# Kernel tuning notes

Hardware: AMD Instinct MI355X
Metric: run time of the kernel (lower is better)

The kernel has to match this reference:

```python
import jax, jax.numpy as jnp
import numpy as np

GAMMA = 1.0
INF_REPLACE = 1e10  # original code replaces inf with 1e10 before logsumexp


def _softmin3(r_diag, r_up, r_left, gamma):
    # softmin over the 3 DP neighbors (stack order matches original: diag, up, left)
    x = jnp.stack([r_diag, r_up, r_left], axis=0)  # (3, B)
    x = jnp.where(jnp.isinf(x), jnp.asarray(INF_REPLACE, x.dtype), x)
    return -gamma * jax.nn.logsumexp(-x / gamma, axis=0)  # (B,)


def _cdist(X, Y):
    # Euclidean pairwise distance, torch.cdist(p=2): (B,N,d),(B,M,d) -> (B,N,M)
    d2 = (jnp.sum(X * X, axis=-1)[:, :, None]
          + jnp.sum(Y * Y, axis=-1)[:, None, :]
          - 2.0 * jnp.einsum('bnd,bmd->bnm', X, Y))
    return jnp.sqrt(jnp.maximum(d2, 0.0))


def _soft_dtw(X, Y, gamma):
    B, N, _ = X.shape
    D = _cdist(X, Y)  # (B, N, N)
    inf = jnp.asarray(jnp.inf, D.dtype)

    # R row 0: [0, inf, inf, ...] per batch
    prev_row0 = jnp.full((B, N + 1), inf, dtype=D.dtype).at[:, 0].set(0.0)

    def row_step(prev_row, d_row):
        # prev_row: (B, N+1) = R[i-1, :]; d_row: (B, N) = D[:, i-1, :]
        xs = (d_row.T, prev_row[:, :-1].T, prev_row[:, 1:].T)  # each (N, B)

        def col_step(r_left, x):
            d, r_diag, r_up = x  # each (B,)
            r = d + _softmin3(r_diag, r_up, r_left, gamma)
            return r, r

        _, row = jax.lax.scan(col_step, jnp.full((B,), inf, dtype=D.dtype), xs)
        new_row = jnp.concatenate([jnp.full((B, 1), inf, dtype=D.dtype), row.T], axis=1)
        return new_row, None

    last_row, _ = jax.lax.scan(row_step, prev_row0, jnp.swapaxes(D, 0, 1))
    return last_row[:, -1]  # R[:, N, N], shape (B,)


def setup_inputs() -> dict:
    key = jax.random.key(0)
    kx, ky = jax.random.split(key)
    B, N, d = 64, 512, 64
    X = jax.random.normal(kx, (B, N, d), dtype=jnp.float32)
    Y = jax.random.normal(ky, (B, N, d), dtype=jnp.float32)
    return {"X": X, "Y": Y}


def reference(X, Y):
    return _soft_dtw(X, Y, GAMMA)
```

## Files before the change

### kernel.cpp

```cpp
#include <hip/hip_runtime.h>
#include <math.h>

#define NB 64
#define NN 512
#define ND 64

#define LOG2E 1.4426950408889634f
#define LN2   0.6931471805599453f
#define RING  16
#define NINF  __int_as_float(0xFF800000u)

typedef __attribute__((ext_vector_type(8))) short  bf16x8;
typedef __attribute__((ext_vector_type(4))) float  f32x4;

static __device__ __forceinline__ unsigned short f2bf(float f) {
    unsigned u = __float_as_uint(f);
    u += 0x7FFFu + ((u >> 16) & 1u);
    return (unsigned short)(u >> 16);
}

__global__ __launch_bounds__(256) void cdist_kernel(const float* __restrict__ X,
                                                    const float* __restrict__ Y,
                                                    unsigned short* __restrict__ Wt) {
    __shared__ unsigned short lX[8][2][512];
    __shared__ unsigned short lY[8][2][512];
    __shared__ float nrmX[128], nrmY[128];

    const int b  = blockIdx.z;
    const int ib = blockIdx.x * 128;
    const int jb = blockIdx.y * 128;
    const int t  = threadIdx.x;

    {
        const int r = t & 127;
        const float* src = (t < 128) ? X + ((size_t)b * NN + ib + r) * ND
                                     : Y + ((size_t)b * NN + jb + r) * ND;
        float v[ND];
        float s = 0.f;
        #pragma unroll
        for (int k = 0; k < ND; k += 4) {
            float4 f = *(const float4*)(src + k);
            v[k] = f.x; v[k + 1] = f.y; v[k + 2] = f.z; v[k + 3] = f.w;
            s += f.x * f.x + f.y * f.y + f.z * f.z + f.w * f.w;
        }
        const int it = r >> 4;
        const int lm = r & 15;
        unsigned short* dst = (t < 128) ? &lX[it][0][0] : &lY[it][0][0];
        #pragma unroll
        for (int h = 0; h < 2; ++h) {
            #pragma unroll
            for (int q = 0; q < 4; ++q) {
                unsigned w[4];
                #pragma unroll
                for (int m = 0; m < 4; ++m) {
                    const int c = h * 32 + q * 8 + 2 * m;
                    w[m] = (unsigned)f2bf(v[c]) | ((unsigned)f2bf(v[c + 1]) << 16);
                }
                uint4 pkt; pkt.x = w[0]; pkt.y = w[1]; pkt.z = w[2]; pkt.w = w[3];
                *(uint4*)(dst + h * 512 + (q * 16 + lm) * 8) = pkt;
            }
        }
        if (t < 128) nrmX[r] = s; else nrmY[r] = s;
    }
    __syncthreads();

    const int wave = t >> 6;
    const int wi   = (wave & 1) * 64;
    const int wj   = (wave >> 1) * 64;
    const int lane = t & 63;
    const int lm   = lane & 15;
    const int quad = lane >> 4;

    f32x4 acc[4][4];
    #pragma unroll
    for (int mt = 0; mt < 4; ++mt)
        #pragma unroll
        for (int nt = 0; nt < 4; ++nt)
            acc[mt][nt] = (f32x4){0.f, 0.f, 0.f, 0.f};

    const int jt0 = wj >> 4;
    const int it0 = wi >> 4;

    #pragma unroll
    for (int h = 0; h < 2; ++h) {
        bf16x8 Af[4], Bf[4];
        #pragma unroll
        for (int mt = 0; mt < 4; ++mt)
            Af[mt] = *(const bf16x8*)&lY[jt0 + mt][h][lane * 8];
        #pragma unroll
        for (int nt = 0; nt < 4; ++nt)
            Bf[nt] = *(const bf16x8*)&lX[it0 + nt][h][lane * 8];
        #pragma unroll
        for (int mt = 0; mt < 4; ++mt)
            #pragma unroll
            for (int nt = 0; nt < 4; ++nt)
                acc[mt][nt] = __builtin_amdgcn_mfma_f32_16x16x32_bf16(
                    Af[mt], Bf[nt], acc[mt][nt], 0, 0, 0);
    }

    float nxv[4];
    float4 nyv[4];
    #pragma unroll
    for (int nt = 0; nt < 4; ++nt)
        nxv[nt] = nrmX[wi + nt * 16 + lm];
    #pragma unroll
    for (int mt = 0; mt < 4; ++mt)
        nyv[mt] = *(const float4*)&nrmY[wj + mt * 16 + quad * 4];

    #pragma unroll
    for (int nt = 0; nt < 4; ++nt) {
        const int i = ib + wi + nt * 16 + lm;
        unsigned short* Drow = Wt + ((size_t)b * NN + i) * NN + jb + wj;
        #pragma unroll
        for (int mt = 0; mt < 4; ++mt) {
            const float* nyp = (const float*)&nyv[mt];
            unsigned a[4];
            #pragma unroll
            for (int r = 0; r < 4; ++r) {
                float d2 = nyp[r] + nxv[nt] - 2.0f * acc[mt][nt][r];
                float w  = __builtin_amdgcn_exp2f(16.0f - LOG2E * sqrtf(fmaxf(d2, 0.f)));
                a[r] = __float_as_uint(w) + 0x8000u;
            }
            uint2 pkt;
            pkt.x = (a[0] >> 16) | (a[1] & 0xFFFF0000u);
            pkt.y = (a[2] >> 16) | (a[3] & 0xFFFF0000u);
            *(uint2*)(Drow + mt * 16 + quad * 4) = pkt;
        }
    }
}

static __device__ __forceinline__ float dpp_shr1(float x, float old) {
    return __int_as_float(__builtin_amdgcn_update_dpp(
        __float_as_int(old), __float_as_int(x), 0x138, 0xf, 0xf, false));
}
static __device__ __forceinline__ float dpp_shl1(float x) {
    return __int_as_float(__builtin_amdgcn_update_dpp(
        0, __float_as_int(x), 0x130, 0xf, 0xf, false));
}

static __device__ __forceinline__ void dtw_step4(
    bool W1, bool DOACT, bool DOGUARD, bool DOCLAMP, bool DOREN,
    int ss, int u, int t, const unsigned short* __restrict__ Wb, int ib,
    uint2* ring, float* L, float& diagHold, float& h, float& Otf,
    float& hbuf, float* __restrict__ h0)
{
    float recvH = dpp_shr1(h, NINF);
    if (W1) {
        recvH = (t == 0) ? hbuf : recvH;
        hbuf  = dpp_shl1(hbuf);
    }
    if (DOACT) { if (ss == t && (t > 0 || W1)) Otf = -recvH; }

    const float up0   = __builtin_amdgcn_exp2f(fminf(recvH + Otf, 80.0f));
    const float diag0 = diagHold;
    diagHold = up0 * 65536.0f;

    const int j = ss - t + 1;
    const uint2 c = ring[u];

    {
        int jn = j + RING;
        if (DOCLAMP) jn = jn < 1 ? 1 : jn;
        ring[u] = *(const uint2*)(Wb + (size_t)(jn - 1) * NN + ib);
    }

    bool act = true;
    if (DOGUARD) act = (j >= 1) && (j <= NN);
    if (act) {
        float dd[4];
        dd[0] = __uint_as_float(c.x << 16);
        dd[1] = __uint_as_float(c.x & 0xFFFF0000u);
        dd[2] = __uint_as_float(c.y << 16);
        dd[3] = __uint_as_float(c.y & 0xFFFF0000u);

        float pre[4], cc[4];
        pre[0] = diag0 + L[0];
        #pragma unroll
        for (int k = 1; k < 4; ++k)
            pre[k] = fmaf(65536.0f, L[k - 1], L[k]);
        #pragma unroll
        for (int k = 0; k < 4; ++k) cc[k] = dd[k] * pre[k];
        float r = up0;
        #pragma unroll
        for (int k = 0; k < 4; ++k) {
            r = fmaf(dd[k], r, cc[k]);
            L[k] = r;
        }

        if (DOREN) {
            float m4 = fmaxf(fmaxf(L[0], L[1]), fmaxf(L[2], L[3]));
            const int   e  = (int)(__float_as_uint(m4) >> 23) - 127;
            const float sc = __uint_as_float((unsigned)(127 - e) << 23);
            #pragma unroll
            for (int k = 0; k < 4; ++k) L[k] *= sc;
            diagHold *= sc;
            Otf -= (float)e;
        }

        h = __builtin_amdgcn_logf(L[3]) - Otf;
        if (!W1) h0[j] = h;
    }
}

static __device__ __forceinline__ void run_chunk(
    bool W1, bool ACT, bool GUARD, bool CLAMP, int base,
    int t, const unsigned short* __restrict__ Wb, int ib,
    uint2* ring, float* L, float& diagHold, float& h, float& Otf,
    float& hbuf, float* __restrict__ h0)
{
    for (int sb = 0; sb < 64; sb += RING)
        #pragma unroll
        for (int u = 0; u < RING; ++u)
            dtw_step4(W1, ACT, GUARD, CLAMP, (u & 1) == 1,
                      base + sb + u, u, t, Wb, ib, ring, L,
                      diagHold, h, Otf, hbuf, h0);
}

__global__ __launch_bounds__(128) void dtw_kernel(const unsigned short* __restrict__ Wt,
                                                  float* __restrict__ out) {
    __shared__ float h0[584];
    const int b    = blockIdx.x;
    const int tid  = threadIdx.x;
    const int t    = tid & 63;
    const int wave = tid >> 6;
    const unsigned short* __restrict__ Wb = Wt + (size_t)b * NN * NN;
    const int ib = wave * 256 + 4 * t;

    float L[4] = {0.f, 0.f, 0.f, 0.f};
    float diagHold = (wave == 0 && t == 0) ? 65536.0f : 0.0f;
    float h = NINF, Otf = 0.0f, hbuf = NINF;

    uint2 ring[RING];
    #pragma unroll
    for (int u = 0; u < RING; ++u) {
        int col = u - t + 1;
        col = col < 1 ? 1 : col;
        ring[u] = *(const uint2*)(Wb + (size_t)(col - 1) * NN + ib);
    }

    for (int wall = 0; wall < 11; ++wall) {
        const int ch = wave ? wall - 2 : wall;
        if (wave == 0) {
            if (ch == 0)
                run_chunk(false, true,  true,  true,  0,      t, Wb, ib, ring, L, diagHold, h, Otf, hbuf, h0);
            else if (ch >= 1 && ch <= 7)
                run_chunk(false, false, false, false, ch*64,  t, Wb, ib, ring, L, diagHold, h, Otf, hbuf, h0);
            else if (ch == 8)
                run_chunk(false, false, true,  false, 512,    t, Wb, ib, ring, L, diagHold, h, Otf, hbuf, h0);
        } else {
            if (ch == 0)
                run_chunk(true,  true,  true,  true,  0,      t, Wb, ib, ring, L, diagHold, h, Otf, hbuf, h0);
            else if (ch >= 1 && ch <= 7)
                run_chunk(true,  false, false, false, ch*64,  t, Wb, ib, ring, L, diagHold, h, Otf, hbuf, h0);
            else if (ch == 8)
                run_chunk(true,  false, true,  false, 512,    t, Wb, ib, ring, L, diagHold, h, Otf, hbuf, h0);
        }
        __syncthreads();
        if (wave && wall >= 1 && wall <= 9)
            hbuf = h0[(wall - 1) * 64 + 1 + t];
    }

    if (wave == 1 && t == 63) out[b] = (16384.0f - h) * LN2;
}

extern "C" void kernel_launch(void* const* d_in, const int* in_sizes, int n_in,
                              void* d_out, int out_size, void* d_ws, size_t ws_size,
                              hipStream_t stream) {
    const float* X = (const float*)d_in[0];
    const float* Y = (const float*)d_in[1];
    float* out = (float*)d_out;

    char* ws = (char*)d_ws;
    unsigned short* Wt = (unsigned short*)(ws);

    cdist_kernel<<<dim3(4, 4, NB), 256, 0, stream>>>(X, Y, Wt);
    dtw_kernel<<<NB, 128, 0, stream>>>(Wt, out);
}
```

Baseline: 145.8 us.

## Fuse cdist and DTW into one persistent kernel with flag-based overlap

Merges the cdist and DTW kernels into one launch. The first 64 blocks run the DTW recurrence and spin on per-batch, per-row-block atomic flags, while the remaining 1024 blocks compute distance tiles and release flags. This lets the DTW wavefront start as soon as its first row-block of weights is ready, rather than waiting for the whole cdist kernel. It uses s_setprio to favour DTW and early tiles. It adds a memset launch and spin-waiting, and it risks deadlock or stalls if DTW blocks occupy slots before the producers are scheduled. DTW blocks are now 256 threads with two idle waves.

```diff
diff --git a/kernel.cpp b/kernel.cpp
--- a/kernel.cpp
+++ b/kernel.cpp
@@ -19,16 +19,114 @@
     return (unsigned short)(u >> 16);
 }
 
-__global__ __launch_bounds__(256) void cdist_kernel(const float* __restrict__ X,
-                                                    const float* __restrict__ Y,
-                                                    unsigned short* __restrict__ Wt) {
-    __shared__ unsigned short lX[8][2][512];
-    __shared__ unsigned short lY[8][2][512];
-    __shared__ float nrmX[128], nrmY[128];
-
-    const int b  = blockIdx.z;
-    const int ib = blockIdx.x * 128;
-    const int jb = blockIdx.y * 128;
+
+static __device__ __forceinline__ float dpp_shr1(float x, float old) {
+    return __int_as_float(__builtin_amdgcn_update_dpp(
+        __float_as_int(old), __float_as_int(x), 0x138, 0xf, 0xf, false));
+}
+static __device__ __forceinline__ float dpp_shl1(float x) {
+    return __int_as_float(__builtin_amdgcn_update_dpp(
+        0, __float_as_int(x), 0x130, 0xf, 0xf, false));
+}
+
+static __device__ __forceinline__ void dtw_step4(
+    bool W1, bool DOACT, bool DOGUARD, bool DOCLAMP, bool DOREN,
+    int ss, int u, int t, const unsigned short* __restrict__ Wb, int ib,
+    uint2* ring, float* L, float& diagHold, float& h, float& Otf,
+    float& hbuf, float* __restrict__ h0)
+{
+    float recvH = dpp_shr1(h, NINF);
+    if (W1) {
+        recvH = (t == 0) ? hbuf : recvH;
+        hbuf  = dpp_shl1(hbuf);
+    }
+    if (DOACT) { if (ss == t && (t > 0 || W1)) Otf = -recvH; }
+
+    const float up0   = __builtin_amdgcn_exp2f(fminf(recvH + Otf, 80.0f));
+    const float diag0 = diagHold;
+    diagHold = up0 * 65536.0f;
+
+    const int j = ss - t + 1;
+    const uint2 c = ring[u];
+
+    {
+        int jn = j + RING;
+        if (DOCLAMP) jn = jn < 1 ? 1 : jn;
+        ring[u] = *(const uint2*)(Wb + (size_t)(jn - 1) * NN + ib);
+    }
+
+    bool act = true;
+    if (DOGUARD) act = (j >= 1) && (j <= NN);
+    if (act) {
+        float dd[4];
+        dd[0] = __uint_as_float(c.x << 16);
+        dd[1] = __uint_as_float(c.x & 0xFFFF0000u);
+        dd[2] = __uint_as_float(c.y << 16);
+        dd[3] = __uint_as_float(c.y & 0xFFFF0000u);
+
+        float pre[4], cc[4];
+        pre[0] = diag0 + L[0];
+        #pragma unroll
+        for (int k = 1; k < 4; ++k)
+            pre[k] = fmaf(65536.0f, L[k - 1], L[k]);
+        #pragma unroll
+        for (int k = 0; k < 4; ++k) cc[k] = dd[k] * pre[k];
+        float r = up0;
+        #pragma unroll
+        for (int k = 0; k < 4; ++k) {
+            r = fmaf(dd[k], r, cc[k]);
+            L[k] = r;
+        }
+
+        if (DOREN) {
+            float m4 = fmaxf(fmaxf(L[0], L[1]), fmaxf(L[2], L[3]));
+            const int   e  = (int)(__float_as_uint(m4) >> 23) - 127;
+            const float sc = __uint_as_float((unsigned)(127 - e) << 23);
+            #pragma unroll
+            for (int k = 0; k < 4; ++k) L[k] *= sc;
+            diagHold *= sc;
+            Otf -= (float)e;
+        }
+
+        h = __builtin_amdgcn_logf(L[3]) - Otf;
+        if (!W1) h0[j] = h;
+    }
+}
+
+static __device__ __forceinline__ void run_chunk(
+    bool W1, bool ACT, bool GUARD, bool CLAMP, int base,
+    int t, const unsigned short* __restrict__ Wb, int ib,
+    uint2* ring, float* L, float& diagHold, float& h, float& Otf,
+    float& hbuf, float* __restrict__ h0)
+{
+    for (int sb = 0; sb < 64; sb += RING)
+        #pragma unroll
+        for (int u = 0; u < RING; ++u)
+            dtw_step4(W1, ACT, GUARD, CLAMP, (u & 1) == 1,
+                      base + sb + u, u, t, Wb, ib, ring, L,
+                      diagHold, h, Otf, hbuf, h0);
+}
+
+static __device__ __forceinline__ void cdist_role(
+    int cb, const float* __restrict__ X, const float* __restrict__ Y,
+    unsigned short* __restrict__ Wt, unsigned int* __restrict__ flags,
+    char* smem)
+{
+    const int bx = cb >> 8;
+    const int by = (cb >> 6) & 3;
+    const int b  = cb & 63;
+
+    if      (bx == 0) __builtin_amdgcn_s_setprio(3);
+    else if (bx == 1) __builtin_amdgcn_s_setprio(2);
+    else if (bx == 2) __builtin_amdgcn_s_setprio(1);
+
+    unsigned short (*lX)[2][512] = (unsigned short (*)[2][512])(smem);
+    unsigned short (*lY)[2][512] = (unsigned short (*)[2][512])(smem + 16384);
+    float* nrmX = (float*)(smem + 32768);
+    float* nrmY = (float*)(smem + 33280);
+
+    const int ib = bx * 128;
+    const int jb = by * 128;
     const int t  = threadIdx.x;
 
     {
@@ -64,9 +162,9 @@
     }
     __syncthreads();
 
-    const int wave = t >> 6;
-    const int wi   = (wave & 1) * 64;
-    const int wj   = (wave >> 1) * 64;
+    const int wv   = t >> 6;
+    const int wi   = (wv & 1) * 64;
+    const int wj   = (wv >> 1) * 64;
     const int lane = t & 63;
     const int lm   = lane & 15;
     const int quad = lane >> 4;
@@ -127,140 +225,92 @@
             *(uint2*)(Drow + mt * 16 + quad * 4) = pkt;
         }
     }
-}
-
-static __device__ __forceinline__ float dpp_shr1(float x, float old) {
-    return __int_as_float(__builtin_amdgcn_update_dpp(
-        __float_as_int(old), __float_as_int(x), 0x138, 0xf, 0xf, false));
-}
-static __device__ __forceinline__ float dpp_shl1(float x) {
-    return __int_as_float(__builtin_amdgcn_update_dpp(
-        0, __float_as_int(x), 0x130, 0xf, 0xf, false));
-}
-
-static __device__ __forceinline__ void dtw_step4(
-    bool W1, bool DOACT, bool DOGUARD, bool DOCLAMP, bool DOREN,
-    int ss, int u, int t, const unsigned short* __restrict__ Wb, int ib,
-    uint2* ring, float* L, float& diagHold, float& h, float& Otf,
-    float& hbuf, float* __restrict__ h0)
+
+    __threadfence();
+    __syncthreads();
+    if (t == 0)
+        __hip_atomic_fetch_add(&flags[b * 4 + bx], 1u,
+                               __ATOMIC_RELEASE, __HIP_MEMORY_SCOPE_AGENT);
+}
+
+static __device__ __forceinline__ void dtw_role(
+    int b, const unsigned short* __restrict__ Wt,
+    unsigned int* __restrict__ flags, float* __restrict__ out, char* smem)
 {
-    float recvH = dpp_shr1(h, NINF);
-    if (W1) {
-        recvH = (t == 0) ? hbuf : recvH;
-        hbuf  = dpp_shl1(hbuf);
-    }
-    if (DOACT) { if (ss == t && (t > 0 || W1)) Otf = -recvH; }
-
-    const float up0   = __builtin_amdgcn_exp2f(fminf(recvH + Otf, 80.0f));
-    const float diag0 = diagHold;
-    diagHold = up0 * 65536.0f;
-
-    const int j = ss - t + 1;
-    const uint2 c = ring[u];
-
-    {
-        int jn = j + RING;
-        if (DOCLAMP) jn = jn < 1 ? 1 : jn;
-        ring[u] = *(const uint2*)(Wb + (size_t)(jn - 1) * NN + ib);
-    }
-
-    bool act = true;
-    if (DOGUARD) act = (j >= 1) && (j <= NN);
-    if (act) {
-        float dd[4];
-        dd[0] = __uint_as_float(c.x << 16);
-        dd[1] = __uint_as_float(c.x & 0xFFFF0000u);
-        dd[2] = __uint_as_float(c.y << 16);
-        dd[3] = __uint_as_float(c.y & 0xFFFF0000u);
-
-        float pre[4], cc[4];
-        pre[0] = diag0 + L[0];
-        #pragma unroll
-        for (int k = 1; k < 4; ++k)
-            pre[k] = fmaf(65536.0f, L[k - 1], L[k]);
-        #pragma unroll
-        for (int k = 0; k < 4; ++k) cc[k] = dd[k] * pre[k];
-        float r = up0;
-        #pragma unroll
-        for (int k = 0; k < 4; ++k) {
-            r = fmaf(dd[k], r, cc[k]);
-            L[k] = r;
-        }
-
-        if (DOREN) {
-            float m4 = fmaxf(fmaxf(L[0], L[1]), fmaxf(L[2], L[3]));
-            const int   e  = (int)(__float_as_uint(m4) >> 23) - 127;
-            const float sc = __uint_as_float((unsigned)(127 - e) << 23);
-            #pragma unroll
-            for (int k = 0; k < 4; ++k) L[k] *= sc;
-            diagHold *= sc;
-            Otf -= (float)e;
-        }
-
-        h = __builtin_amdgcn_logf(L[3]) - Otf;
-        if (!W1) h0[j] = h;
-    }
-}
-
-static __device__ __forceinline__ void run_chunk(
-    bool W1, bool ACT, bool GUARD, bool CLAMP, int base,
-    int t, const unsigned short* __restrict__ Wb, int ib,
-    uint2* ring, float* L, float& diagHold, float& h, float& Otf,
-    float& hbuf, float* __restrict__ h0)
-{
-    for (int sb = 0; sb < 64; sb += RING)
-        #pragma unroll
-        for (int u = 0; u < RING; ++u)
-            dtw_step4(W1, ACT, GUARD, CLAMP, (u & 1) == 1,
-                      base + sb + u, u, t, Wb, ib, ring, L,
-                      diagHold, h, Otf, hbuf, h0);
-}
-
-__global__ __launch_bounds__(128) void dtw_kernel(const unsigned short* __restrict__ Wt,
-                                                  float* __restrict__ out) {
-    __shared__ float h0[584];
-    const int b    = blockIdx.x;
+    float* h0 = (float*)smem;
     const int tid  = threadIdx.x;
     const int t    = tid & 63;
     const int wave = tid >> 6;
+    __builtin_amdgcn_s_setprio(3);
     const unsigned short* __restrict__ Wb = Wt + (size_t)b * NN * NN;
-    const int ib = wave * 256 + 4 * t;
+    const int ib = (wave & 1) * 256 + 4 * t;
 
     float L[4] = {0.f, 0.f, 0.f, 0.f};
     float diagHold = (wave == 0 && t == 0) ? 65536.0f : 0.0f;
     float h = NINF, Otf = 0.0f, hbuf = NINF;
-
     uint2 ring[RING];
-    #pragma unroll
-    for (int u = 0; u < RING; ++u) {
-        int col = u - t + 1;
-        col = col < 1 ? 1 : col;
-        ring[u] = *(const uint2*)(Wb + (size_t)(col - 1) * NN + ib);
+
+    if (tid == 0)
+        while (__hip_atomic_load(&flags[b * 4 + 0], __ATOMIC_ACQUIRE,
+                                 __HIP_MEMORY_SCOPE_AGENT) < 4u)
+            __builtin_amdgcn_s_sleep(8);
+    __syncthreads();
+    int have = 0;
+
+    if (wave < 2) {
+        #pragma unroll
+        for (int u = 0; u < RING; ++u) {
+            int col = u - t + 1;
+            col = col < 1 ? 1 : col;
+            ring[u] = *(const uint2*)(Wb + (size_t)(col - 1) * NN + ib);
+        }
     }
 
     for (int wall = 0; wall < 11; ++wall) {
-        const int ch = wave ? wall - 2 : wall;
+        int need = (wall * 64 + 79) >> 7;
+        need = need > 3 ? 3 : need;
+        if (need != have) {
+            if (tid == 0)
+                for (int x = have + 1; x <= need; ++x)
+                    while (__hip_atomic_load(&flags[b * 4 + x], __ATOMIC_ACQUIRE,
+                                             __HIP_MEMORY_SCOPE_AGENT) < 4u)
+                        __builtin_amdgcn_s_sleep(8);
+            __syncthreads();
+            have = need;
+        }
         if (wave == 0) {
+            if (wall == 0)
+                run_chunk(false, true,  true,  true,  0,       t, Wb, ib, ring, L, diagHold, h, Otf, hbuf, h0);
+            else if (wall <= 7)
+                run_chunk(false, false, false, false, wall*64, t, Wb, ib, ring, L, diagHold, h, Otf, hbuf, h0);
+            else if (wall == 8)
+                run_chunk(false, false, true,  false, 512,     t, Wb, ib, ring, L, diagHold, h, Otf, hbuf, h0);
+        } else if (wave == 1) {
+            const int ch = wall - 2;
             if (ch == 0)
-                run_chunk(false, true,  true,  true,  0,      t, Wb, ib, ring, L, diagHold, h, Otf, hbuf, h0);
+                run_chunk(true,  true,  true,  true,  0,       t, Wb, ib, ring, L, diagHold, h, Otf, hbuf, h0);
             else if (ch >= 1 && ch <= 7)
-                run_chunk(false, false, false, false, ch*64,  t, Wb, ib, ring, L, diagHold, h, Otf, hbuf, h0);
+                run_chunk(true,  false, false, false, ch*64,   t, Wb, ib, ring, L, diagHold, h, Otf, hbuf, h0);
             else if (ch == 8)
-                run_chunk(false, false, true,  false, 512,    t, Wb, ib, ring, L, diagHold, h, Otf, hbuf, h0);
-        } else {
-            if (ch == 0)
-                run_chunk(true,  true,  true,  true,  0,      t, Wb, ib, ring, L, diagHold, h, Otf, hbuf, h0);
-            else if (ch >= 1 && ch <= 7)
-                run_chunk(true,  false, false, false, ch*64,  t, Wb, ib, ring, L, diagHold, h, Otf, hbuf, h0);
-            else if (ch == 8)
-                run_chunk(true,  false, true,  false, 512,    t, Wb, ib, ring, L, diagHold, h, Otf, hbuf, h0);
+                run_chunk(true,  false, true,  false, 512,     t, Wb, ib, ring, L, diagHold, h, Otf, hbuf, h0);
         }
         __syncthreads();
-        if (wave && wall >= 1 && wall <= 9)
+        if (wave == 1 && wall >= 1 && wall <= 9)
             hbuf = h0[(wall - 1) * 64 + 1 + t];
     }
 
     if (wave == 1 && t == 63) out[b] = (16384.0f - h) * LN2;
+}
+
+__global__ __launch_bounds__(256) void fused_kernel(const float* __restrict__ X,
+                                                    const float* __restrict__ Y,
+                                                    unsigned short* __restrict__ Wt,
+                                                    unsigned int* __restrict__ flags,
+                                                    float* __restrict__ out) {
+    __shared__ __align__(16) char smem[33792];
+    const int bid = blockIdx.x;
+    if (bid < NB) dtw_role(bid, Wt, flags, out, smem);
+    else          cdist_role(bid - NB, X, Y, Wt, flags, smem);
 }
 
 extern "C" void kernel_launch(void* const* d_in, const int* in_sizes, int n_in,
@@ -271,8 +321,9 @@
     float* out = (float*)d_out;
 
     char* ws = (char*)d_ws;
-    unsigned short* Wt = (unsigned short*)(ws);
-
-    cdist_kernel<<<dim3(4, 4, NB), 256, 0, stream>>>(X, Y, Wt);
-    dtw_kernel<<<NB, 128, 0, stream>>>(Wt, out);
-}
+    unsigned short* Wt = (unsigned short*)ws;
+    unsigned int* flags = (unsigned int*)(ws + 41943040);
+
+    hipMemsetAsync(flags, 0, NB * 4 * sizeof(unsigned int), stream);
+    fused_kernel<<<dim3(NB + 1024), 256, 0, stream>>>(X, Y, Wt, flags, out);
+}
```

Result: slower. 293.4 us (+101.2%).
